# Optimization experiments

Measured on AMD Instinct MI355X. Metric: run time of the kernel, lower is better.

The kernel has to match this reference:

```python
import jax, jax.numpy as jnp
import numpy as np


def setup_inputs() -> dict:
    key = jax.random.key(0)
    k1, k2, k3 = jax.random.split(key, 3)
    B, Cin, Cout, K, H, W = 32, 128, 128, 4, 112, 112
    x = jax.random.normal(k1, (B, Cin, H, W), dtype=jnp.float32)
    # Conv2d 1x1 weights: [K, out_ch, in_ch] (kernel dims of size 1 squeezed)
    expert_w = jax.random.normal(k2, (K, Cout, Cin), dtype=jnp.float32) * (1.0 / np.sqrt(Cin))
    gate_w = jax.random.normal(k3, (K, Cin), dtype=jnp.float32) * (1.0 / np.sqrt(Cin))
    gate_b = jnp.zeros((K,), dtype=jnp.float32)
    return {"x": x, "expert_w": expert_w, "gate_w": gate_w, "gate_b": gate_b}


def reference(x, expert_w, gate_w, gate_b):
    # Gate: global average pool -> 1x1 conv -> softmax over K
    pooled = jnp.mean(x, axis=(2, 3))                      # [B, Cin]
    logits = pooled @ gate_w.T + gate_b                    # [B, K]
    g = jax.nn.softmax(logits, axis=1)                     # [B, K]
    # Combine expert weights per sample (math-equivalent to sum_k g_k * conv_k(x))
    w_b = jnp.einsum('bk,koi->boi', g, expert_w)           # [B, Cout, Cin]
    out = jnp.einsum('boi,bihw->bohw', w_b, x)             # [B, Cout, H, W]
    return out
```

## Files before the change

### kernel.cpp

```cpp
#include <hip/hip_runtime.h>
#include <hip/hip_bf16.h>
#include <stdint.h>

#define B_     32
#define CIN    128
#define COUT   128
#define KEXP   4
#define HW_    12544
#define NCHUNK 196
#define NPT    392

typedef __attribute__((ext_vector_type(8))) short bf16x8;
typedef __attribute__((ext_vector_type(4))) float f32x4;
typedef __attribute__((ext_vector_type(16))) float f32x16;

static __device__ __forceinline__ short f2bf(float f) {
    __hip_bfloat16 h = __float2bfloat16(f);
    return __builtin_bit_cast(short, h);
}


__global__ __launch_bounds__(256) void prep_kernel(const float* __restrict__ x,
                                                   short* __restrict__ xbf2,
                                                   float* __restrict__ partial) {
    const int b  = blockIdx.y;
    const int cx = blockIdx.x;
    const int p0 = cx * 64;
    const int t  = threadIdx.x;
    const int pg  = t & 15;
    const int cg8 = t >> 4;

    const float* __restrict__ xr = x + (size_t)b * CIN * HW_
                                 + (size_t)(cg8 * 8) * HW_ + p0 + pg * 4;
    f32x4 va[8];
    #pragma unroll
    for (int i = 0; i < 8; ++i)
        va[i] = *(const f32x4*)(xr + (size_t)i * HW_);

    float ps[8];
    #pragma unroll
    for (int i = 0; i < 8; ++i) ps[i] = (va[i][0] + va[i][1]) + (va[i][2] + va[i][3]);
    #pragma unroll
    for (int m = 1; m < 16; m <<= 1) {
        #pragma unroll
        for (int i = 0; i < 8; ++i) ps[i] += __shfl_xor(ps[i], m, 64);
    }
    if (pg == 0) {
        float* pdst = partial + ((size_t)b * NCHUNK + cx) * CIN + cg8 * 8;
        f32x4 v0 = {ps[0], ps[1], ps[2], ps[3]};
        f32x4 v1 = {ps[4], ps[5], ps[6], ps[7]};
        *(f32x4*)pdst = v0;
        *(f32x4*)(pdst + 4) = v1;
    }

    short* __restrict__ xd = xbf2
        + ((size_t)(b * NPT + cx * 2 + (pg >> 3)) * 8 + (cg8 >> 1)) * 512
        + ((cg8 & 1) * 32 + (pg & 7) * 4) * 8;
    #pragma unroll
    for (int jj = 0; jj < 4; ++jj) {
        bf16x8 pk;
        #pragma unroll
        for (int i = 0; i < 8; ++i) pk[i] = f2bf(va[i][jj]);
        *(bf16x8*)(xd + jj * 8) = pk;
    }
}

__global__ __launch_bounds__(256) void gate2_kernel(const float* __restrict__ partial,
                                                    const float* __restrict__ gate_w,
                                                    const float* __restrict__ gate_b,
                                                    const float* __restrict__ expert_w,
                                                    short* __restrict__ wmix2) {
    const int b = blockIdx.x;
    const int t = threadIdx.x;
    __shared__ float psum[2][CIN];
    __shared__ float pl[CIN];
    {
        const int cin  = t & 127;
        const int half = t >> 7;
        float s = 0.f;
        const float* pp = partial + (size_t)b * NCHUNK * CIN + (size_t)(half * 98) * CIN + cin;
        #pragma unroll 7
        for (int c = 0; c < 98; ++c) s += pp[(size_t)c * CIN];
        psum[half][cin] = s;
    }
    __syncthreads();
    if (t < CIN) pl[t] = (psum[0][t] + psum[1][t]) * (1.0f / HW_);
    __syncthreads();

    const int wid = t >> 6, lane = t & 63;
    __shared__ float logits[KEXP];
    __shared__ float gsh[KEXP];
    {
        float s = pl[lane] * gate_w[wid * CIN + lane]
                + pl[64 + lane] * gate_w[wid * CIN + 64 + lane];
        #pragma unroll
        for (int off = 32; off > 0; off >>= 1) s += __shfl_down(s, off, 64);
        if (lane == 0) logits[wid] = s + gate_b[wid];
    }
    __syncthreads();
    if (t == 0) {
        float m = fmaxf(fmaxf(logits[0], logits[1]), fmaxf(logits[2], logits[3]));
        float e0 = expf(logits[0] - m), e1 = expf(logits[1] - m);
        float e2 = expf(logits[2] - m), e3 = expf(logits[3] - m);
        float inv = 1.f / (e0 + e1 + e2 + e3);
        gsh[0] = e0 * inv; gsh[1] = e1 * inv; gsh[2] = e2 * inv; gsh[3] = e3 * inv;
    }
    __syncthreads();
    const float g0 = gsh[0], g1 = gsh[1], g2 = gsh[2], g3 = gsh[3];
    for (int idx = t; idx < COUT * CIN; idx += 256) {
        float w = g0 * expert_w[idx]
                + g1 * expert_w[COUT * CIN + idx]
                + g2 * expert_w[2 * COUT * CIN + idx]
                + g3 * expert_w[3 * COUT * CIN + idx];
        const int o = idx >> 7, c = idx & 127;
        const int dst = ((b * 4 + (o >> 5)) * 8 + (c >> 4)) * 512
                      + (((c >> 3) & 1) * 32 + (o & 31)) * 8 + (c & 7);
        wmix2[dst] = f2bf(w);
    }
}

__global__ __launch_bounds__(256, 4) void conv3_kernel(const short* __restrict__ xbf2,
                                                       const short* __restrict__ wmix2,
                                                       float* __restrict__ out) {
    __shared__ short wlds[4 * 8 * 512];
    const int t = threadIdx.x;

    const int b = (B_ - 1) - blockIdx.y;

    const int orig = blockIdx.x;
    const int xcd = orig & 7, idx = orig >> 3;
    const int wgid = (xcd < 1 ? xcd * 7 : 7 + (xcd - 1) * 6) + idx;
    const int ug = 48 - wgid;

    {
        const short* __restrict__ wsrc = wmix2 + (size_t)b * 16384;
        #pragma unroll
        for (int pass = 0; pass < 8; ++pass) {
            uint4 v = *(const uint4*)(wsrc + pass * 2048 + t * 8);
            *(uint4*)(wlds + pass * 2048 + t * 8) = v;
        }
    }

    const int wave = t >> 6;
    const int lane = t & 63;
    const int pt0  = ug * 8 + wave * 2;

    const short* __restrict__ xb = xbf2 + ((size_t)(b * NPT + pt0) * 8) * 512 + lane * 8;
    bf16x8 b0[8], b1[8];
    #pragma unroll
    for (int f = 0; f < 8; ++f) b0[f] = *(const bf16x8*)(xb + f * 512);
    #pragma unroll
    for (int f = 0; f < 8; ++f) b1[f] = *(const bf16x8*)(xb + (8 + f) * 512);

    __syncthreads();

    const int rowadd = 4 * (lane >> 5);
    float* __restrict__ ob0 = out + (size_t)b * COUT * HW_ + pt0 * 32 + (lane & 31);
    float* __restrict__ ob1 = ob0 + 32;

    #pragma unroll
    for (int ct = 0; ct < 4; ++ct) {
        f32x16 a0, a1;
        #pragma unroll
        for (int r = 0; r < 16; ++r) { a0[r] = 0.f; a1[r] = 0.f; }

        const short* __restrict__ wl = wlds + (ct * 8) * 512 + lane * 8;
        #pragma unroll
        for (int f = 0; f < 8; ++f) {
            bf16x8 afrag = *(const bf16x8*)(wl + f * 512);
            a0 = __builtin_amdgcn_mfma_f32_32x32x16_bf16(afrag, b0[f], a0, 0, 0, 0);
            a1 = __builtin_amdgcn_mfma_f32_32x32x16_bf16(afrag, b1[f], a1, 0, 0, 0);
        }

        #pragma unroll
        for (int r = 0; r < 16; ++r) {
            const int cout = ct * 32 + (r & 3) + 8 * (r >> 2) + rowadd;
            __builtin_nontemporal_store(a0[r], ob0 + (size_t)cout * HW_);
            __builtin_nontemporal_store(a1[r], ob1 + (size_t)cout * HW_);
        }
    }
}


__global__ __launch_bounds__(256) void pool_kernel(const float* __restrict__ x,
                                                   float* __restrict__ pooled) {
    const int row = blockIdx.x;
    const float4* __restrict__ x4 = (const float4*)(x + (size_t)row * HW_);
    const int t = threadIdx.x;
    float s = 0.f;
    for (int idx = t; idx < HW_ / 4; idx += 256) {
        float4 v = x4[idx];
        s += (v.x + v.y) + (v.z + v.w);
    }
    #pragma unroll
    for (int off = 32; off > 0; off >>= 1) s += __shfl_down(s, off, 64);
    __shared__ float wsum[4];
    if ((t & 63) == 0) wsum[t >> 6] = s;
    __syncthreads();
    if (t == 0) pooled[row] = (wsum[0] + wsum[1] + wsum[2] + wsum[3]) * (1.0f / HW_);
}

__global__ __launch_bounds__(256) void gate_kernel(const float* __restrict__ pooled,
                                                   const float* __restrict__ gate_w,
                                                   const float* __restrict__ gate_b,
                                                   const float* __restrict__ expert_w,
                                                   short* __restrict__ wmix) {
    const int b = blockIdx.x;
    const int t = threadIdx.x;
    const int wid = t >> 6, lane = t & 63;
    __shared__ float logits[KEXP];
    __shared__ float gsh[KEXP];
    {
        float p0 = pooled[b * CIN + lane];
        float p1 = pooled[b * CIN + 64 + lane];
        float s = p0 * gate_w[wid * CIN + lane] + p1 * gate_w[wid * CIN + 64 + lane];
        #pragma unroll
        for (int off = 32; off > 0; off >>= 1) s += __shfl_down(s, off, 64);
        if (lane == 0) logits[wid] = s + gate_b[wid];
    }
    __syncthreads();
    if (t == 0) {
        float m = fmaxf(fmaxf(logits[0], logits[1]), fmaxf(logits[2], logits[3]));
        float e0 = expf(logits[0] - m), e1 = expf(logits[1] - m);
        float e2 = expf(logits[2] - m), e3 = expf(logits[3] - m);
        float inv = 1.f / (e0 + e1 + e2 + e3);
        gsh[0] = e0 * inv; gsh[1] = e1 * inv; gsh[2] = e2 * inv; gsh[3] = e3 * inv;
    }
    __syncthreads();
    const float g0 = gsh[0], g1 = gsh[1], g2 = gsh[2], g3 = gsh[3];
    for (int idx = t; idx < COUT * CIN; idx += 256) {
        float w = g0 * expert_w[idx]
                + g1 * expert_w[COUT * CIN + idx]
                + g2 * expert_w[2 * COUT * CIN + idx]
                + g3 * expert_w[3 * COUT * CIN + idx];
        wmix[b * COUT * CIN + idx] = f2bf(w);
    }
}

__global__ __launch_bounds__(256, 4) void conv_fb_kernel(const float* __restrict__ x,
                                                         const short* __restrict__ wmix,
                                                         float* __restrict__ out) {
    __shared__ char wlds[COUT * 256];
    __shared__ char xlds[64 * 256];
    const int b  = blockIdx.y;
    const int p0 = blockIdx.x * 64;
    const int t  = threadIdx.x;

    {
        const uint4* __restrict__ wsrc = (const uint4*)(wmix + (size_t)b * COUT * CIN);
        #pragma unroll
        for (int pass = 0; pass < 8; ++pass) {
            int o  = (t >> 4) + pass * 16;
            int i4 = t & 15;
            uint4 v = wsrc[o * 16 + i4];
            *(uint4*)(wlds + o * 256 + ((i4 ^ (o & 15)) << 4)) = v;
        }
    }
    {
        const int pg = t & 15;
        const int cg = t >> 4;
        #pragma unroll
        for (int p = 0; p < 2; ++p) {
            const int cin0 = p * 64 + cg * 4;
            const float* xrow = x + (size_t)b * CIN * HW_ + (size_t)cin0 * HW_ + p0 + pg * 4;
            float va[4][4];
            #pragma unroll
            for (int i = 0; i < 4; ++i) {
                float4 v = *(const float4*)(xrow + (size_t)i * HW_);
                va[i][0] = v.x; va[i][1] = v.y; va[i][2] = v.z; va[i][3] = v.w;
            }
            #pragma unroll
            for (int j = 0; j < 4; ++j) {
                const int pix = pg * 4 + j;
                uint32_t lo = (uint32_t)(ushort)f2bf(va[0][j]) | ((uint32_t)(ushort)f2bf(va[1][j]) << 16);
                uint32_t hi = (uint32_t)(ushort)f2bf(va[2][j]) | ((uint32_t)(ushort)f2bf(va[3][j]) << 16);
                int byte = (pix * 256 + cin0 * 2) ^ ((pix & 7) << 4);
                uint2 w2; w2.x = lo; w2.y = hi;
                *(uint2*)(xlds + byte) = w2;
            }
        }
    }

    const int wave = t >> 6;
    const int lane = t & 63;
    const int n = lane & 15;
    const int h = lane >> 4;

    __syncthreads();

    bf16x8 xfrag[4];
    {
        const int pixl = wave * 16 + n;
        #pragma unroll
        for (int kk = 0; kk < 4; ++kk) {
            int byte = (pixl * 256 + kk * 64 + h * 16) ^ ((pixl & 7) << 4);
            xfrag[kk] = *(const bf16x8*)(xlds + byte);
        }
    }

    f32x4 acc[8];
    #pragma unroll
    for (int ot = 0; ot < 8; ++ot) acc[ot] = (f32x4){0.f, 0.f, 0.f, 0.f};

    #pragma unroll
    for (int ot = 0; ot < 8; ++ot) {
        const int o = ot * 16 + n;
        #pragma unroll
        for (int kk = 0; kk < 4; ++kk) {
            bf16x8 wfrag = *(const bf16x8*)(wlds + o * 256 + (((kk * 4 + h) ^ n) << 4));
            acc[ot] = __builtin_amdgcn_mfma_f32_16x16x32_bf16(xfrag[kk], wfrag, acc[ot], 0, 0, 0);
        }
    }

    float* __restrict__ ob = out + (size_t)b * COUT * HW_ + p0 + wave * 16 + h * 4;
    #pragma unroll
    for (int ot = 0; ot < 8; ++ot)
        __builtin_nontemporal_store(acc[ot], (f32x4*)(ob + (size_t)(ot * 16 + n) * HW_));
}

extern "C" void kernel_launch(void* const* d_in, const int* in_sizes, int n_in,
                              void* d_out, int out_size, void* d_ws, size_t ws_size,
                              hipStream_t stream) {
    const float* x        = (const float*)d_in[0];
    const float* expert_w = (const float*)d_in[1];
    const float* gate_w   = (const float*)d_in[2];
    const float* gate_b   = (const float*)d_in[3];
    float* out = (float*)d_out;

    const size_t PARTIAL_B = (size_t)B_ * NCHUNK * CIN * 4;
    const size_t WMIX_B    = (size_t)B_ * COUT * CIN * 2;
    const size_t XBF_B     = (size_t)B_ * HW_ * CIN * 2;
    const size_t NEED      = PARTIAL_B + WMIX_B + XBF_B;

    if (ws_size >= NEED) {
        float* partial = (float*)d_ws;
        short* wmix2   = (short*)((char*)d_ws + PARTIAL_B);
        short* xbf2    = (short*)((char*)d_ws + PARTIAL_B + WMIX_B);

        prep_kernel<<<dim3(NCHUNK, B_), 256, 0, stream>>>(x, xbf2, partial);
        gate2_kernel<<<dim3(B_), 256, 0, stream>>>(partial, gate_w, gate_b, expert_w, wmix2);
        conv3_kernel<<<dim3(49, B_), 256, 0, stream>>>(xbf2, wmix2, out);
    } else {
        float* pooled = (float*)d_ws;
        short* wmix   = (short*)((char*)d_ws + 16384);
        pool_kernel<<<dim3(B_ * CIN), 256, 0, stream>>>(x, pooled);
        gate_kernel<<<dim3(B_), 256, 0, stream>>>(pooled, gate_w, gate_b, expert_w, wmix);
        conv_fb_kernel<<<dim3(HW_ / 64, B_), 256, 0, stream>>>(x, wmix, out);
    }
}
```

Measured before the change: 129.9 us.

## Process batch in groups through a two-slot ring buffer for cache residency

Splits prep, gate and conv into four batch groups of 8 that are launched in an interleaved order and share a two-slot bf16 ring buffer instead of one full-size converted copy of x. The aim is to keep each converted slot resident in the last-level cache between the prep and conv kernels, cutting HBM traffic for the intermediate. In exchange it adds more kernel launches, gives smaller grids with worse tail utilization, and drops the XCD-aware block remapping.

```diff
diff --git a/kernel.cpp b/kernel.cpp
--- a/kernel.cpp
+++ b/kernel.cpp
@@ -9,6 +9,9 @@
 #define HW_    12544
 #define NCHUNK 196
 #define NPT    392
+#define GB     8
+#define NG     4
+#define SLOT_SHORTS ((size_t)GB * NPT * 8 * 512)
 
 typedef __attribute__((ext_vector_type(8))) short bf16x8;
 typedef __attribute__((ext_vector_type(4))) float f32x4;
@@ -20,10 +23,12 @@
 }
 
 
-__global__ __launch_bounds__(256) void prep_kernel(const float* __restrict__ x,
-                                                   short* __restrict__ xbf2,
-                                                   float* __restrict__ partial) {
-    const int b  = blockIdx.y;
+__global__ __launch_bounds__(256) void prep4_kernel(const float* __restrict__ x,
+                                                    short* __restrict__ xslot,
+                                                    float* __restrict__ partial,
+                                                    int b0) {
+    const int bl = blockIdx.y;
+    const int b  = b0 + bl;
     const int cx = blockIdx.x;
     const int p0 = cx * 64;
     const int t  = threadIdx.x;
@@ -53,8 +58,8 @@
         *(f32x4*)(pdst + 4) = v1;
     }
 
-    short* __restrict__ xd = xbf2
-        + ((size_t)(b * NPT + cx * 2 + (pg >> 3)) * 8 + (cg8 >> 1)) * 512
+    short* __restrict__ xd = xslot
+        + ((size_t)(bl * NPT + cx * 2 + (pg >> 3)) * 8 + (cg8 >> 1)) * 512
         + ((cg8 & 1) * 32 + (pg & 7) * 4) * 8;
     #pragma unroll
     for (int jj = 0; jj < 4; ++jj) {
@@ -65,12 +70,13 @@
     }
 }
 
-__global__ __launch_bounds__(256) void gate2_kernel(const float* __restrict__ partial,
+__global__ __launch_bounds__(256) void gate4_kernel(const float* __restrict__ partial,
                                                     const float* __restrict__ gate_w,
                                                     const float* __restrict__ gate_b,
                                                     const float* __restrict__ expert_w,
-                                                    short* __restrict__ wmix2) {
-    const int b = blockIdx.x;
+                                                    short* __restrict__ wmix2,
+                                                    int b0) {
+    const int b = b0 + blockIdx.x;
     const int t = threadIdx.x;
     __shared__ float psum[2][CIN];
     __shared__ float pl[CIN];
@@ -119,18 +125,14 @@
     }
 }
 
-__global__ __launch_bounds__(256, 4) void conv3_kernel(const short* __restrict__ xbf2,
+__global__ __launch_bounds__(256, 4) void conv4_kernel(const short* __restrict__ xslot,
                                                        const short* __restrict__ wmix2,
-                                                       float* __restrict__ out) {
+                                                       float* __restrict__ out,
+                                                       int b0) {
     __shared__ short wlds[4 * 8 * 512];
-    const int t = threadIdx.x;
-
-    const int b = (B_ - 1) - blockIdx.y;
-
-    const int orig = blockIdx.x;
-    const int xcd = orig & 7, idx = orig >> 3;
-    const int wgid = (xcd < 1 ? xcd * 7 : 7 + (xcd - 1) * 6) + idx;
-    const int ug = 48 - wgid;
+    const int bl = blockIdx.y;
+    const int b  = b0 + bl;
+    const int t  = threadIdx.x;
 
     {
         const short* __restrict__ wsrc = wmix2 + (size_t)b * 16384;
@@ -143,14 +145,14 @@
 
     const int wave = t >> 6;
     const int lane = t & 63;
-    const int pt0  = ug * 8 + wave * 2;
-
-    const short* __restrict__ xb = xbf2 + ((size_t)(b * NPT + pt0) * 8) * 512 + lane * 8;
-    bf16x8 b0[8], b1[8];
-    #pragma unroll
-    for (int f = 0; f < 8; ++f) b0[f] = *(const bf16x8*)(xb + f * 512);
-    #pragma unroll
-    for (int f = 0; f < 8; ++f) b1[f] = *(const bf16x8*)(xb + (8 + f) * 512);
+    const int pt0  = blockIdx.x * 8 + wave * 2;
+
+    const short* __restrict__ xb = xslot + ((size_t)(bl * NPT + pt0) * 8) * 512 + lane * 8;
+    bf16x8 b0f[8], b1f[8];
+    #pragma unroll
+    for (int f = 0; f < 8; ++f) b0f[f] = *(const bf16x8*)(xb + f * 512);
+    #pragma unroll
+    for (int f = 0; f < 8; ++f) b1f[f] = *(const bf16x8*)(xb + (8 + f) * 512);
 
     __syncthreads();
 
@@ -168,8 +170,8 @@
         #pragma unroll
         for (int f = 0; f < 8; ++f) {
             bf16x8 afrag = *(const bf16x8*)(wl + f * 512);
-            a0 = __builtin_amdgcn_mfma_f32_32x32x16_bf16(afrag, b0[f], a0, 0, 0, 0);
-            a1 = __builtin_amdgcn_mfma_f32_32x32x16_bf16(afrag, b1[f], a1, 0, 0, 0);
+            a0 = __builtin_amdgcn_mfma_f32_32x32x16_bf16(afrag, b0f[f], a0, 0, 0, 0);
+            a1 = __builtin_amdgcn_mfma_f32_32x32x16_bf16(afrag, b1f[f], a1, 0, 0, 0);
         }
 
         #pragma unroll
@@ -329,17 +331,35 @@
 
     const size_t PARTIAL_B = (size_t)B_ * NCHUNK * CIN * 4;
     const size_t WMIX_B    = (size_t)B_ * COUT * CIN * 2;
-    const size_t XBF_B     = (size_t)B_ * HW_ * CIN * 2;
-    const size_t NEED      = PARTIAL_B + WMIX_B + XBF_B;
+    const size_t RING_B    = 2 * SLOT_SHORTS * 2;
+    const size_t NEED      = PARTIAL_B + WMIX_B + RING_B;
 
     if (ws_size >= NEED) {
         float* partial = (float*)d_ws;
         short* wmix2   = (short*)((char*)d_ws + PARTIAL_B);
-        short* xbf2    = (short*)((char*)d_ws + PARTIAL_B + WMIX_B);
-
-        prep_kernel<<<dim3(NCHUNK, B_), 256, 0, stream>>>(x, xbf2, partial);
-        gate2_kernel<<<dim3(B_), 256, 0, stream>>>(partial, gate_w, gate_b, expert_w, wmix2);
-        conv3_kernel<<<dim3(49, B_), 256, 0, stream>>>(xbf2, wmix2, out);
+        short* ring    = (short*)((char*)d_ws + PARTIAL_B + WMIX_B);
+
+        auto PREP = [&](int g) {
+            prep4_kernel<<<dim3(NCHUNK, GB), 256, 0, stream>>>(
+                x, ring + (size_t)(g & 1) * SLOT_SHORTS, partial, g * GB);
+        };
+        auto GATE = [&](int g) {
+            gate4_kernel<<<dim3(GB), 256, 0, stream>>>(
+                partial, gate_w, gate_b, expert_w, wmix2, g * GB);
+        };
+        auto CONV = [&](int g) {
+            conv4_kernel<<<dim3(49, GB), 256, 0, stream>>>(
+                ring + (size_t)(g & 1) * SLOT_SHORTS, wmix2, out, g * GB);
+        };
+
+        PREP(0); GATE(0);
+        PREP(1); GATE(1);
+        CONV(0);
+        PREP(2); GATE(2);
+        CONV(1);
+        PREP(3); GATE(3);
+        CONV(2);
+        CONV(3);
     } else {
         float* pooled = (float*)d_ws;
         short* wmix   = (short*)((char*)d_ws + 16384);
```

Measured after the change: 199.0 us. +53.2%, slower.

## Fuse gate computation and expert weight mixing into the conv kernel

Applied to the files above, without the earlier changes.

Removes the separate gate kernel and the wmix2 workspace. Each conv workgroup now reduces the pooled partials, computes the softmax gate and mixes the expert weights directly into LDS, after issuing its x-fragment loads so those loads overlap the gate work. This saves one kernel launch and a global round trip for the mixed weights. The cost is that the gate and weight-mixing work is repeated in every one of the 49 workgroups per sample, and occupancy is lowered to 3 waves-per-EU bound.

```diff
diff --git a/kernel.cpp b/kernel.cpp
--- a/kernel.cpp
+++ b/kernel.cpp
@@ -65,15 +65,36 @@
     }
 }
 
-__global__ __launch_bounds__(256) void gate2_kernel(const float* __restrict__ partial,
-                                                    const float* __restrict__ gate_w,
-                                                    const float* __restrict__ gate_b,
-                                                    const float* __restrict__ expert_w,
-                                                    short* __restrict__ wmix2) {
-    const int b = blockIdx.x;
-    const int t = threadIdx.x;
+__global__ __launch_bounds__(256, 3) void convg_kernel(const short* __restrict__ xbf2,
+                                                       const float* __restrict__ partial,
+                                                       const float* __restrict__ gate_w,
+                                                       const float* __restrict__ gate_b,
+                                                       const float* __restrict__ expert_w,
+                                                       float* __restrict__ out) {
+    __shared__ short wlds[4 * 8 * 512];
     __shared__ float psum[2][CIN];
     __shared__ float pl[CIN];
+    __shared__ float logits[KEXP], gsh[KEXP];
+
+    const int t = threadIdx.x;
+    const int b = (B_ - 1) - blockIdx.y;
+
+    const int orig = blockIdx.x;
+    const int xcd = orig & 7, idx = orig >> 3;
+    const int wgid = (xcd < 1 ? xcd * 7 : 7 + (xcd - 1) * 6) + idx;
+    const int ug = 48 - wgid;
+
+    const int wave = t >> 6;
+    const int lane = t & 63;
+    const int pt0  = ug * 8 + wave * 2;
+
+    const short* __restrict__ xb = xbf2 + ((size_t)(b * NPT + pt0) * 8) * 512 + lane * 8;
+    bf16x8 b0f[8], b1f[8];
+    #pragma unroll
+    for (int f = 0; f < 8; ++f) b0f[f] = *(const bf16x8*)(xb + f * 512);
+    #pragma unroll
+    for (int f = 0; f < 8; ++f) b1f[f] = *(const bf16x8*)(xb + (8 + f) * 512);
+
     {
         const int cin  = t & 127;
         const int half = t >> 7;
@@ -86,11 +107,8 @@
     __syncthreads();
     if (t < CIN) pl[t] = (psum[0][t] + psum[1][t]) * (1.0f / HW_);
     __syncthreads();
-
-    const int wid = t >> 6, lane = t & 63;
-    __shared__ float logits[KEXP];
-    __shared__ float gsh[KEXP];
-    {
+    {
+        const int wid = t >> 6;
         float s = pl[lane] * gate_w[wid * CIN + lane]
                 + pl[64 + lane] * gate_w[wid * CIN + 64 + lane];
         #pragma unroll
@@ -106,52 +124,19 @@
         gsh[0] = e0 * inv; gsh[1] = e1 * inv; gsh[2] = e2 * inv; gsh[3] = e3 * inv;
     }
     __syncthreads();
-    const float g0 = gsh[0], g1 = gsh[1], g2 = gsh[2], g3 = gsh[3];
-    for (int idx = t; idx < COUT * CIN; idx += 256) {
-        float w = g0 * expert_w[idx]
-                + g1 * expert_w[COUT * CIN + idx]
-                + g2 * expert_w[2 * COUT * CIN + idx]
-                + g3 * expert_w[3 * COUT * CIN + idx];
-        const int o = idx >> 7, c = idx & 127;
-        const int dst = ((b * 4 + (o >> 5)) * 8 + (c >> 4)) * 512
-                      + (((c >> 3) & 1) * 32 + (o & 31)) * 8 + (c & 7);
-        wmix2[dst] = f2bf(w);
-    }
-}
-
-__global__ __launch_bounds__(256, 4) void conv3_kernel(const short* __restrict__ xbf2,
-                                                       const short* __restrict__ wmix2,
-                                                       float* __restrict__ out) {
-    __shared__ short wlds[4 * 8 * 512];
-    const int t = threadIdx.x;
-
-    const int b = (B_ - 1) - blockIdx.y;
-
-    const int orig = blockIdx.x;
-    const int xcd = orig & 7, idx = orig >> 3;
-    const int wgid = (xcd < 1 ? xcd * 7 : 7 + (xcd - 1) * 6) + idx;
-    const int ug = 48 - wgid;
-
-    {
-        const short* __restrict__ wsrc = wmix2 + (size_t)b * 16384;
-        #pragma unroll
-        for (int pass = 0; pass < 8; ++pass) {
-            uint4 v = *(const uint4*)(wsrc + pass * 2048 + t * 8);
-            *(uint4*)(wlds + pass * 2048 + t * 8) = v;
-        }
-    }
-
-    const int wave = t >> 6;
-    const int lane = t & 63;
-    const int pt0  = ug * 8 + wave * 2;
-
-    const short* __restrict__ xb = xbf2 + ((size_t)(b * NPT + pt0) * 8) * 512 + lane * 8;
-    bf16x8 b0[8], b1[8];
-    #pragma unroll
-    for (int f = 0; f < 8; ++f) b0[f] = *(const bf16x8*)(xb + f * 512);
-    #pragma unroll
-    for (int f = 0; f < 8; ++f) b1[f] = *(const bf16x8*)(xb + (8 + f) * 512);
-
+    {
+        const float g0 = gsh[0], g1 = gsh[1], g2 = gsh[2], g3 = gsh[3];
+        for (int idx2 = t; idx2 < COUT * CIN; idx2 += 256) {
+            float w = g0 * expert_w[idx2]
+                    + g1 * expert_w[COUT * CIN + idx2]
+                    + g2 * expert_w[2 * COUT * CIN + idx2]
+                    + g3 * expert_w[3 * COUT * CIN + idx2];
+            const int o = idx2 >> 7, c = idx2 & 127;
+            const int dst = ((o >> 5) * 8 + (c >> 4)) * 512
+                          + (((c >> 3) & 1) * 32 + (o & 31)) * 8 + (c & 7);
+            wlds[dst] = f2bf(w);
+        }
+    }
     __syncthreads();
 
     const int rowadd = 4 * (lane >> 5);
@@ -168,10 +153,9 @@
         #pragma unroll
         for (int f = 0; f < 8; ++f) {
             bf16x8 afrag = *(const bf16x8*)(wl + f * 512);
-            a0 = __builtin_amdgcn_mfma_f32_32x32x16_bf16(afrag, b0[f], a0, 0, 0, 0);
-            a1 = __builtin_amdgcn_mfma_f32_32x32x16_bf16(afrag, b1[f], a1, 0, 0, 0);
-        }
-
+            a0 = __builtin_amdgcn_mfma_f32_32x32x16_bf16(afrag, b0f[f], a0, 0, 0, 0);
+            a1 = __builtin_amdgcn_mfma_f32_32x32x16_bf16(afrag, b1f[f], a1, 0, 0, 0);
+        }
         #pragma unroll
         for (int r = 0; r < 16; ++r) {
             const int cout = ct * 32 + (r & 3) + 8 * (r >> 2) + rowadd;
@@ -328,18 +312,16 @@
     float* out = (float*)d_out;
 
     const size_t PARTIAL_B = (size_t)B_ * NCHUNK * CIN * 4;
-    const size_t WMIX_B    = (size_t)B_ * COUT * CIN * 2;
     const size_t XBF_B     = (size_t)B_ * HW_ * CIN * 2;
-    const size_t NEED      = PARTIAL_B + WMIX_B + XBF_B;
+    const size_t NEED      = PARTIAL_B + XBF_B;
 
     if (ws_size >= NEED) {
         float* partial = (float*)d_ws;
-        short* wmix2   = (short*)((char*)d_ws + PARTIAL_B);
-        short* xbf2    = (short*)((char*)d_ws + PARTIAL_B + WMIX_B);
+        short* xbf2    = (short*)((char*)d_ws + PARTIAL_B);
 
         prep_kernel<<<dim3(NCHUNK, B_), 256, 0, stream>>>(x, xbf2, partial);
-        gate2_kernel<<<dim3(B_), 256, 0, stream>>>(partial, gate_w, gate_b, expert_w, wmix2);
-        conv3_kernel<<<dim3(49, B_), 256, 0, stream>>>(xbf2, wmix2, out);
+        convg_kernel<<<dim3(49, B_), 256, 0, stream>>>(xbf2, partial, gate_w,
+                                                       gate_b, expert_w, out);
     } else {
         float* pooled = (float*)d_ws;
         short* wmix   = (short*)((char*)d_ws + 16384);
```

Measured after the change: 130.6 us. Within noise of the previous version (+0.5%).
